# Kernel optimization log

Measured on AMD Instinct MI355X. Metric: run time of the kernel, lower is better.

Reference implementation:

```python
import jax, jax.numpy as jnp
import numpy as np

R = 32          # voxel resolution
EPS = 0.0       # normalization eps


def setup_inputs() -> dict:
    key = jax.random.key(0)
    k1, k2 = jax.random.split(key)
    B, D, N = 16, 64, 32768
    features = jax.random.normal(k1, (B, D, N), dtype=jnp.float32)
    coords = jax.random.normal(k2, (B, 3, N), dtype=jnp.float32)
    return {"features": features, "coords": coords}


def reference(features, coords):
    """features: (B, D, N), coords: (B, 3, N).
    Returns (voxel_features (B, D, R, R, R), norm_coords (B, 3, N))."""
    B, D, N = features.shape
    r = R

    # --- normalize coords into [0, r-1] (torch detaches coords; fwd math identical) ---
    nc = coords - coords.mean(axis=2, keepdims=True)                    # center
    norm = jnp.linalg.norm(nc, axis=1, keepdims=True)                   # (B,1,N)
    max_norm = norm.max(axis=2, keepdims=True)                          # (B,1,1)
    nc = nc / (max_norm * 2.0 + EPS) + 0.5
    norm_coords = jnp.clip(nc * r, 0, r - 1)                            # (B,3,N)
    vox = jnp.round(norm_coords).astype(jnp.int32)                      # (B,3,N)

    # --- scatter-mean features into r^3 voxels (avg_voxelize) ---
    idx = vox[:, 0] * (r * r) + vox[:, 1] * r + vox[:, 2]               # (B,N) in [0, r^3)
    flat_idx = (idx + jnp.arange(B, dtype=jnp.int32)[:, None] * (r ** 3)).reshape(-1)  # (B*N,)
    flat_feat = features.transpose(0, 2, 1).reshape(B * N, D)           # (B*N, D)

    sums = jax.ops.segment_sum(flat_feat, flat_idx, num_segments=B * r ** 3)   # (B*r^3, D)
    cnt = jax.ops.segment_sum(jnp.ones((B * N,), dtype=features.dtype),
                              flat_idx, num_segments=B * r ** 3)               # (B*r^3,)
    avg = sums / jnp.maximum(cnt, 1.0)[:, None]                          # empty voxels -> 0

    vox_feat = avg.reshape(B, r ** 3, D).transpose(0, 2, 1).reshape(B, D, r, r, r)
    return vox_feat, norm_coords
```

## Files before the change

kernel.cpp:

```cpp
#include <hip/hip_runtime.h>

#define RES 32
#define R3 (RES * RES * RES)

__device__ __forceinline__ void fadd_native(float* p, float v) {
    unsafeAtomicAdd(p, v);
}

__global__ void sums_kernel(const float* __restrict__ coords,
                            float* __restrict__ accum, int N) {
    const int b = blockIdx.y;
    const int stride = gridDim.x * blockDim.x;
    const float* cb = coords + (size_t)b * 3 * N;
    const int nvec = N >> 2;
    const float4* c0 = (const float4*)cb;
    const float4* c1 = (const float4*)(cb + N);
    const float4* c2 = (const float4*)(cb + 2 * N);

    float s0 = 0.f, s1 = 0.f, s2 = 0.f;
    for (int n = blockIdx.x * blockDim.x + threadIdx.x; n < nvec; n += stride) {
        float4 a = c0[n]; s0 += (a.x + a.y) + (a.z + a.w);
        float4 c = c1[n]; s1 += (c.x + c.y) + (c.z + c.w);
        float4 d = c2[n]; s2 += (d.x + d.y) + (d.z + d.w);
    }
    if (blockIdx.x == 0 && threadIdx.x == 0) {
        for (int n = nvec << 2; n < N; ++n) {
            s0 += cb[n]; s1 += cb[N + n]; s2 += cb[2 * N + n];
        }
    }
    for (int off = 32; off; off >>= 1) {
        s0 += __shfl_down(s0, off);
        s1 += __shfl_down(s1, off);
        s2 += __shfl_down(s2, off);
    }
    __shared__ float r0[4], r1[4], r2[4];
    const int lane = threadIdx.x & 63, wv = threadIdx.x >> 6;
    if (lane == 0) { r0[wv] = s0; r1[wv] = s1; r2[wv] = s2; }
    __syncthreads();
    if (threadIdx.x == 0) {
        float t0 = 0.f, t1 = 0.f, t2 = 0.f;
        const int nw = blockDim.x >> 6;
        for (int w = 0; w < nw; ++w) { t0 += r0[w]; t1 += r1[w]; t2 += r2[w]; }
        fadd_native(&accum[b * 4 + 0], t0);
        fadd_native(&accum[b * 4 + 1], t1);
        fadd_native(&accum[b * 4 + 2], t2);
    }
}

__global__ void maxn_kernel(const float* __restrict__ coords,
                            const float* __restrict__ accum,
                            unsigned* __restrict__ maxsq, int N) {
    const int b = blockIdx.y;
    const int stride = gridDim.x * blockDim.x;
    const float* cb = coords + (size_t)b * 3 * N;
    const float m0 = accum[b * 4 + 0] / (float)N;
    const float m1 = accum[b * 4 + 1] / (float)N;
    const float m2 = accum[b * 4 + 2] / (float)N;
    const int nvec = N >> 2;
    const float4* c0 = (const float4*)cb;
    const float4* c1 = (const float4*)(cb + N);
    const float4* c2 = (const float4*)(cb + 2 * N);

    float mx = 0.f;
    for (int n = blockIdx.x * blockDim.x + threadIdx.x; n < nvec; n += stride) {
        float4 a = c0[n], c = c1[n], d = c2[n];
        a.x -= m0; a.y -= m0; a.z -= m0; a.w -= m0;
        c.x -= m1; c.y -= m1; c.z -= m1; c.w -= m1;
        d.x -= m2; d.y -= m2; d.z -= m2; d.w -= m2;
        mx = fmaxf(mx, a.x * a.x + c.x * c.x + d.x * d.x);
        mx = fmaxf(mx, a.y * a.y + c.y * c.y + d.y * d.y);
        mx = fmaxf(mx, a.z * a.z + c.z * c.z + d.z * d.z);
        mx = fmaxf(mx, a.w * a.w + c.w * c.w + d.w * d.w);
    }
    if (blockIdx.x == 0 && threadIdx.x == 0) {
        for (int n = nvec << 2; n < N; ++n) {
            float a = cb[n] - m0, c = cb[N + n] - m1, d = cb[2 * N + n] - m2;
            mx = fmaxf(mx, a * a + c * c + d * d);
        }
    }
    for (int off = 32; off; off >>= 1) mx = fmaxf(mx, __shfl_down(mx, off));
    __shared__ float r0[4];
    const int lane = threadIdx.x & 63, wv = threadIdx.x >> 6;
    if (lane == 0) r0[wv] = mx;
    __syncthreads();
    if (threadIdx.x == 0) {
        const int nw = blockDim.x >> 6;
        for (int w = 0; w < nw; ++w) mx = fmaxf(mx, r0[w]);
        atomicMax(&maxsq[b], __float_as_uint(mx));
    }
}

__global__ void point_kernel(const float* __restrict__ coords,
                             const float* __restrict__ accum,
                             const unsigned* __restrict__ maxsq,
                             float* __restrict__ nc_out,
                             int* __restrict__ idx_out,
                             int* __restrict__ counts, int N) {
    const int n4 = blockIdx.x * blockDim.x + threadIdx.x;
    const int b = blockIdx.y;
    const int nvec = (N + 3) >> 2;
    if (n4 >= nvec) return;

    const float* cb = coords + (size_t)b * 3 * N;
    const float m0 = accum[b * 4 + 0] / (float)N;
    const float m1 = accum[b * 4 + 1] / (float)N;
    const float m2 = accum[b * 4 + 2] / (float)N;
    const float denom = 2.0f * sqrtf(__uint_as_float(maxsq[b]));
    float* ncb = nc_out + (size_t)b * 3 * N;
    int* irow = idx_out + (size_t)b * N;
    int* crow = counts + (size_t)b * R3;

    const int n0 = n4 << 2;
    if (n0 + 3 < N) {
        float4 a = *(const float4*)(cb + n0);
        float4 c = *(const float4*)(cb + N + n0);
        float4 d = *(const float4*)(cb + 2 * N + n0);
        float4 v0, v1, v2;
        int4 id;
        #define PROC(comp)                                                        \
        {                                                                         \
            float x = (a.comp - m0) / denom + 0.5f;                               \
            float y = (c.comp - m1) / denom + 0.5f;                               \
            float z = (d.comp - m2) / denom + 0.5f;                               \
            v0.comp = fminf(fmaxf(x * (float)RES, 0.f), (float)(RES - 1));        \
            v1.comp = fminf(fmaxf(y * (float)RES, 0.f), (float)(RES - 1));        \
            v2.comp = fminf(fmaxf(z * (float)RES, 0.f), (float)(RES - 1));        \
            id.comp = (int)rintf(v0.comp) * RES * RES                             \
                    + (int)rintf(v1.comp) * RES + (int)rintf(v2.comp);            \
        }
        PROC(x) PROC(y) PROC(z) PROC(w)
        #undef PROC
        *(float4*)(ncb + n0) = v0;
        *(float4*)(ncb + N + n0) = v1;
        *(float4*)(ncb + 2 * N + n0) = v2;
        *(int4*)(irow + n0) = id;
        atomicAdd(&crow[id.x], 1);
        atomicAdd(&crow[id.y], 1);
        atomicAdd(&crow[id.z], 1);
        atomicAdd(&crow[id.w], 1);
    } else {
        for (int n = n0; n < N; ++n) {
            float x = (cb[n] - m0) / denom + 0.5f;
            float y = (cb[N + n] - m1) / denom + 0.5f;
            float z = (cb[2 * N + n] - m2) / denom + 0.5f;
            float v0 = fminf(fmaxf(x * (float)RES, 0.f), (float)(RES - 1));
            float v1 = fminf(fmaxf(y * (float)RES, 0.f), (float)(RES - 1));
            float v2 = fminf(fmaxf(z * (float)RES, 0.f), (float)(RES - 1));
            ncb[n] = v0; ncb[N + n] = v1; ncb[2 * N + n] = v2;
            int id = (int)rintf(v0) * RES * RES + (int)rintf(v1) * RES + (int)rintf(v2);
            irow[n] = id;
            atomicAdd(&crow[id], 1);
        }
    }
}

__global__ __launch_bounds__(1024) void reduce_kernel(
        const float* __restrict__ feats,
        const int* __restrict__ idx,
        const int* __restrict__ counts,
        float* __restrict__ vox, int D, int N) {
    const int d = blockIdx.x;
    const int b = blockIdx.y;
    const int tid = threadIdx.x;

    __shared__ float acc[R3];
    {
        float4* a4 = (float4*)acc;
        const float4 z = make_float4(0.f, 0.f, 0.f, 0.f);
        for (int v = tid; v < (R3 >> 2); v += blockDim.x) a4[v] = z;
    }
    __syncthreads();

    const float* frow = feats + ((size_t)b * D + d) * N;
    const int* irow = idx + (size_t)b * N;
    const int nvec = N >> 2;
    const float4* f4 = (const float4*)frow;
    const int4* i4 = (const int4*)irow;
    for (int n = tid; n < nvec; n += blockDim.x) {
        float4 f = f4[n];
        int4 i = i4[n];
        fadd_native(&acc[i.x], f.x);
        fadd_native(&acc[i.y], f.y);
        fadd_native(&acc[i.z], f.z);
        fadd_native(&acc[i.w], f.w);
    }
    if (tid == 0) {
        for (int n = nvec << 2; n < N; ++n) fadd_native(&acc[irow[n]], frow[n]);
    }
    __syncthreads();

    const int* crow = counts + (size_t)b * R3;
    float* vrow = vox + ((size_t)b * D + d) * R3;
    const int4* c4 = (const int4*)crow;
    float4* v4 = (float4*)vrow;
    for (int v = tid; v < (R3 >> 2); v += blockDim.x) {
        int4 c = c4[v];
        float4 a = ((const float4*)acc)[v];
        a.x /= (float)(c.x > 1 ? c.x : 1);
        a.y /= (float)(c.y > 1 ? c.y : 1);
        a.z /= (float)(c.z > 1 ? c.z : 1);
        a.w /= (float)(c.w > 1 ? c.w : 1);
        v4[v] = a;
    }
}

extern "C" void kernel_launch(void* const* d_in, const int* in_sizes, int n_in,
                              void* d_out, int out_size, void* d_ws, size_t ws_size,
                              hipStream_t stream) {
    const float* feats  = (const float*)d_in[0];
    const float* coords = (const float*)d_in[1];
    float* out = (float*)d_out;

    const int D = (int)(3LL * in_sizes[0] / in_sizes[1]);
    const int B = (int)((long long)(out_size - in_sizes[1]) / ((long long)D * R3));
    const int N = in_sizes[1] / (3 * B);

    float* vox_out = out;
    float* nc_out  = out + (size_t)B * D * R3;

    float*    accum  = (float*)d_ws;
    unsigned* maxsq  = (unsigned*)((char*)d_ws + 1024);
    int*      counts = (int*)((char*)d_ws + 4096);
    int*      idx    = (int*)((char*)d_ws + 4096 + (size_t)B * R3 * sizeof(int));

    hipMemsetAsync(d_ws, 0, 4096 + (size_t)B * R3 * sizeof(int), stream);

    sums_kernel <<<dim3(8, B), dim3(256), 0, stream>>>(coords, accum, N);
    maxn_kernel <<<dim3(8, B), dim3(256), 0, stream>>>(coords, accum, maxsq, N);

    const int nvec = (N + 3) >> 2;
    point_kernel<<<dim3((nvec + 255) / 256, B), dim3(256), 0, stream>>>(
        coords, accum, maxsq, nc_out, idx, counts, N);

    reduce_kernel<<<dim3(D, B), dim3(1024), 0, stream>>>(
        feats, idx, counts, vox_out, D, N);
}
```

Measured before the change: 396.9 us.

## Split voxel reduction into two halves per block to halve shared memory

The reduce kernel now launches two blocks per (d,b), each owning half of the voxel range, so shared accumulator usage drops from 128KB to 64KB and more blocks can be resident per CU. Each block still reads the full feature and index rows, doubling global reads of those arrays, and filters atomics by range. The scatter loop also gains a one-step software prefetch, and the final division uses fast __fdividef, which may differ slightly in rounding.

```diff
diff --git a/kernel.cpp b/kernel.cpp
--- a/kernel.cpp
+++ b/kernel.cpp
@@ -2,6 +2,7 @@
 
 #define RES 32
 #define R3 (RES * RES * RES)
+#define HALF (R3 / 2)
 
 __device__ __forceinline__ void fadd_native(float* p, float v) {
     unsafeAtomicAdd(p, v);
@@ -154,52 +155,74 @@
     }
 }
 
-__global__ __launch_bounds__(1024) void reduce_kernel(
+__global__ __launch_bounds__(1024, 8) void reduce_kernel(
         const float* __restrict__ feats,
         const int* __restrict__ idx,
         const int* __restrict__ counts,
         float* __restrict__ vox, int D, int N) {
     const int d = blockIdx.x;
     const int b = blockIdx.y;
+    const int lo = (int)blockIdx.z * HALF;
     const int tid = threadIdx.x;
 
-    __shared__ float acc[R3];
+    __shared__ float acc[HALF];
     {
         float4* a4 = (float4*)acc;
         const float4 z = make_float4(0.f, 0.f, 0.f, 0.f);
-        for (int v = tid; v < (R3 >> 2); v += blockDim.x) a4[v] = z;
+        for (int v = tid; v < (HALF >> 2); v += 1024) a4[v] = z;
     }
     __syncthreads();
 
     const float* frow = feats + ((size_t)b * D + d) * N;
     const int* irow = idx + (size_t)b * N;
     const int nvec = N >> 2;
-    const float4* f4 = (const float4*)frow;
-    const int4* i4 = (const int4*)irow;
-    for (int n = tid; n < nvec; n += blockDim.x) {
-        float4 f = f4[n];
-        int4 i = i4[n];
-        fadd_native(&acc[i.x], f.x);
-        fadd_native(&acc[i.y], f.y);
-        fadd_native(&acc[i.z], f.z);
-        fadd_native(&acc[i.w], f.w);
-    }
+    const float4* f4p = (const float4*)frow;
+    const int4* i4p = (const int4*)irow;
+
+    #define SCATTER4(f, i)                                                       \
+    {                                                                            \
+        unsigned a0 = (unsigned)((i).x - lo);                                    \
+        if (a0 < (unsigned)HALF) fadd_native(&acc[a0], (f).x);                   \
+        unsigned a1 = (unsigned)((i).y - lo);                                    \
+        if (a1 < (unsigned)HALF) fadd_native(&acc[a1], (f).y);                   \
+        unsigned a2 = (unsigned)((i).z - lo);                                    \
+        if (a2 < (unsigned)HALF) fadd_native(&acc[a2], (f).z);                   \
+        unsigned a3 = (unsigned)((i).w - lo);                                    \
+        if (a3 < (unsigned)HALF) fadd_native(&acc[a3], (f).w);                   \
+    }
+
+    if (tid < nvec) {
+        float4 f = f4p[tid];
+        int4   i = i4p[tid];
+        for (int n = tid + 1024; n < nvec; n += 1024) {
+            float4 fn = f4p[n];
+            int4   in_ = i4p[n];
+            SCATTER4(f, i)
+            f = fn; i = in_;
+        }
+        SCATTER4(f, i)
+    }
+    #undef SCATTER4
+
     if (tid == 0) {
-        for (int n = nvec << 2; n < N; ++n) fadd_native(&acc[irow[n]], frow[n]);
-    }
-    __syncthreads();
-
-    const int* crow = counts + (size_t)b * R3;
-    float* vrow = vox + ((size_t)b * D + d) * R3;
+        for (int n = nvec << 2; n < N; ++n) {
+            unsigned a = (unsigned)(irow[n] - lo);
+            if (a < (unsigned)HALF) fadd_native(&acc[a], frow[n]);
+        }
+    }
+    __syncthreads();
+
+    const int* crow = counts + (size_t)b * R3 + lo;
+    float* vrow = vox + ((size_t)b * D + d) * R3 + lo;
     const int4* c4 = (const int4*)crow;
     float4* v4 = (float4*)vrow;
-    for (int v = tid; v < (R3 >> 2); v += blockDim.x) {
+    for (int v = tid; v < (HALF >> 2); v += 1024) {
         int4 c = c4[v];
         float4 a = ((const float4*)acc)[v];
-        a.x /= (float)(c.x > 1 ? c.x : 1);
-        a.y /= (float)(c.y > 1 ? c.y : 1);
-        a.z /= (float)(c.z > 1 ? c.z : 1);
-        a.w /= (float)(c.w > 1 ? c.w : 1);
+        a.x = __fdividef(a.x, (float)(c.x > 1 ? c.x : 1));
+        a.y = __fdividef(a.y, (float)(c.y > 1 ? c.y : 1));
+        a.z = __fdividef(a.z, (float)(c.z > 1 ? c.z : 1));
+        a.w = __fdividef(a.w, (float)(c.w > 1 ? c.w : 1));
         v4[v] = a;
     }
 }
@@ -232,6 +255,6 @@
     point_kernel<<<dim3((nvec + 255) / 256, B), dim3(256), 0, stream>>>(
         coords, accum, maxsq, nc_out, idx, counts, N);
 
-    reduce_kernel<<<dim3(D, B), dim3(1024), 0, stream>>>(
+    reduce_kernel<<<dim3(D, B, 2), dim3(1024), 0, stream>>>(
         feats, idx, counts, vox_out, D, N);
 }
```

Measured after the change: 383.2 us. -3.5%, faster.
